# Optimization experiments

Hardware: AMD Instinct MI355X
Metric: run time of the kernel (lower is better)

## Reference

```python
import jax, jax.numpy as jnp
import numpy as np

Z_DIM = 2
N_STEPS = 4  # fixed-step RK4 stand-in for adaptive dopri5 over t in [0, 1]


def _mlp(t, z, W1, b1, W2, b2, W3, b3):
    # get_z_dot: concat time column before every layer, softplus between layers
    h = z
    params = ((W1, b1), (W2, b2), (W3, b3))
    for i, (W, b) in enumerate(params):
        tcol = jnp.full((h.shape[0], 1), t, dtype=h.dtype)
        h = jnp.concatenate([tcol, h], axis=1) @ W.T + b
        if i < len(params) - 1:
            h = jax.nn.softplus(h)
    return h


def _dynamics(t, z, params):
    # z_dot = NN(t, z); exact divergence = trace of dz_dot/dz via JVPs with basis vectors
    f = lambda zz: _mlp(t, zz, *params)
    div = jnp.zeros((z.shape[0],), dtype=z.dtype)
    z_dot = None
    for i in range(Z_DIM):
        e = jnp.zeros_like(z).at[:, i].set(1.0)
        primal, jv = jax.jvp(f, (z,), (e,))
        z_dot = primal
        div = div + jv[:, i]
    return z_dot, -div[:, None]


def _integrate(z, delta_logpz, params):
    dt = 1.0 / N_STEPS
    f = lambda tt, zz: _dynamics(tt, zz, params)

    def step(carry, i):
        zc, lc = carry
        t = i * dt
        k1z, k1l = f(t, zc)
        k2z, k2l = f(t + 0.5 * dt, zc + 0.5 * dt * k1z)
        k3z, k3l = f(t + 0.5 * dt, zc + 0.5 * dt * k2z)
        k4z, k4l = f(t + dt, zc + dt * k3z)
        zn = zc + (dt / 6.0) * (k1z + 2.0 * k2z + 2.0 * k3z + k4z)
        ln = lc + (dt / 6.0) * (k1l + 2.0 * k2l + 2.0 * k3l + k4l)
        return (zn, ln), None

    (zf, lf), _ = jax.lax.scan(step, (z, delta_logpz), jnp.arange(N_STEPS, dtype=z.dtype))
    return zf, lf


def setup_inputs() -> dict:
    key = jax.random.key(0)
    ks = jax.random.split(key, 4)
    B = 262144
    z = jax.random.normal(ks[0], (B, Z_DIM), dtype=jnp.float32)
    delta_logpz = jnp.zeros((B, 1), dtype=jnp.float32)
    # Linear layers: in_dim + 1 for time column
    W1 = jax.random.normal(ks[1], (64, Z_DIM + 1), dtype=jnp.float32) * (1.0 / np.sqrt(Z_DIM + 1))
    b1 = jnp.zeros((64,), dtype=jnp.float32)
    W2 = jax.random.normal(ks[2], (64, 64 + 1), dtype=jnp.float32) * (1.0 / np.sqrt(65))
    b2 = jnp.zeros((64,), dtype=jnp.float32)
    W3 = jax.random.normal(ks[3], (Z_DIM, 64 + 1), dtype=jnp.float32) * (1.0 / np.sqrt(65))
    b3 = jnp.zeros((Z_DIM,), dtype=jnp.float32)
    return {"z": z, "delta_logpz": delta_logpz, "W1": W1, "b1": b1, "W2": W2, "b2": b2, "W3": W3, "b3": b3}


def reference(z, delta_logpz, W1, b1, W2, b2, W3, b3):
    params = (W1, b1, W2, b2, W3, b3)
    return _integrate(z, delta_logpz, params)
```

## Files before the change

kernel.cpp:

```cpp
#include <hip/hip_runtime.h>

#define HDIM 64
#define NSTEPS 4

typedef __attribute__((ext_vector_type(4))) float f32x4;
typedef __attribute__((ext_vector_type(8))) short bf16x8;
typedef unsigned int uint;

union FragU { uint u[4]; uint4 u4; bf16x8 v; };

__device__ inline uint cvt_pk_bf16(float a, float b) {
  uint d;
  asm("v_cvt_pk_bf16_f32 %0, %1, %2" : "=v"(d) : "v"(a), "v"(b));
  return d;
}
__device__ inline float lo_bf16_f32(uint p) { return __builtin_bit_cast(float, p << 16); }
__device__ inline float hi_bf16_f32(uint p) { return __builtin_bit_cast(float, p & 0xFFFF0000u); }

__device__ inline unsigned short rne_bf16u(float x) {
  uint u = __builtin_bit_cast(uint, x);
  uint r = u + 0x7FFFu + ((u >> 16) & 1u);
  return (unsigned short)(r >> 16);
}
__device__ inline float bf16f(unsigned short h) { return __builtin_bit_cast(float, ((uint)h) << 16); }

__device__ inline float row_sum16(float x) {
  int v = __builtin_bit_cast(int, x);
  x += __builtin_bit_cast(float, __builtin_amdgcn_update_dpp(0, v, 0x128, 0xF, 0xF, true));
  v = __builtin_bit_cast(int, x);
  x += __builtin_bit_cast(float, __builtin_amdgcn_update_dpp(0, v, 0x124, 0xF, 0xF, true));
  v = __builtin_bit_cast(int, x);
  x += __builtin_bit_cast(float, __builtin_amdgcn_update_dpp(0, v, 0x122, 0xF, 0xF, true));
  v = __builtin_bit_cast(int, x);
  x += __builtin_bit_cast(float, __builtin_amdgcn_update_dpp(0, v, 0x121, 0xF, 0xF, true));
  return x;
}

__device__ inline void pack2(float x0, float x1, uint& H, uint& L) {
  uint h = cvt_pk_bf16(x0, x1);
  H = h;
  L = cvt_pk_bf16(x0 - lo_bf16_f32(h), x1 - hi_bf16_f32(h));
}

__device__ inline void l1chain(float4 par, float base, float s0, float s1,
                               float& sp, float& sg) {
  float a = fmaf(par.y, s0, fmaf(par.z, s1, base));
  float ex = __expf(-fabsf(a));
  float rc = __builtin_amdgcn_rcpf(1.0f + ex);
  sg = (a >= 0.f ? 1.0f : ex) * rc;
  sp = fmaxf(a, 0.f) + __logf(1.0f + ex);
}


__global__ void ffjord_prep(const float* __restrict__ W1, const float* __restrict__ b1,
                            const float* __restrict__ W2, const float* __restrict__ b2,
                            const float* __restrict__ W3, const float* __restrict__ b3,
                            float* __restrict__ ws) {
  int tid = threadIdx.x;
  uint* wsu = (uint*)ws;
  for (int e2 = tid; e2 < 8192; e2 += 256) {
    int mat = e2 >> 11;
    int rem = e2 & 2047;
    int fr  = rem >> 8;
    int l   = (rem >> 2) & 63;
    int d   = rem & 3;
    int kt = fr >> 2, nt = fr & 3;
    int g = l >> 4, cc = l & 15;
    int k0 = kt * 32 + g * 8 + 2 * d;
    int j  = nt * 16 + cc;
    float v0, v1;
    if (mat < 2) {
      v0 = W2[j * 65 + k0 + 1];
      v1 = W2[j * 65 + k0 + 2];
    } else {
      float p0 = W1[k0 * 3 + 1] * W3[j + 1] + W1[k0 * 3 + 2] * W3[65 + j + 1];
      float p1 = W1[(k0 + 1) * 3 + 1] * W3[j + 1] + W1[(k0 + 1) * 3 + 2] * W3[65 + j + 1];
      v0 = p0 * W2[j * 65 + k0 + 1];
      v1 = p1 * W2[j * 65 + k0 + 2];
    }
    unsigned short h0 = rne_bf16u(v0), h1 = rne_bf16u(v1);
    if (mat & 1) {
      h0 = rne_bf16u(v0 - bf16f(rne_bf16u(v0)));
      h1 = rne_bf16u(v1 - bf16f(rne_bf16u(v1)));
    }
    wsu[e2] = (uint)h0 | ((uint)h1 << 16);
  }
  if (tid < HDIM) {
    ws[8192 + tid * 4 + 0] = W1[tid * 3 + 0];
    ws[8192 + tid * 4 + 1] = W1[tid * 3 + 1];
    ws[8192 + tid * 4 + 2] = W1[tid * 3 + 2];
    ws[8192 + tid * 4 + 3] = b1[tid];
    ws[8448 + tid * 2 + 0] = W2[tid * 65 + 0];
    ws[8448 + tid * 2 + 1] = b2[tid];
    ws[8576 + tid * 2 + 0] = W3[tid + 1];
    ws[8576 + tid * 2 + 1] = W3[65 + tid + 1];
  }
  if (tid == 0) {
    ws[8704] = W3[0];
    ws[8705] = W3[65];
    ws[8706] = b3[0];
    ws[8707] = b3[1];
  }
}

__global__ __launch_bounds__(256, 2) void ffjord_main(
    const float* __restrict__ z_in, const float* __restrict__ dlp_in,
    const float* __restrict__ ws, float* __restrict__ out, int B) {
  __shared__ uint4 fragLds[2048];
  __shared__ float4 l1Lds[64];
  __shared__ float2 c2Lds[64];
  __shared__ float2 l3Lds[64];
  __shared__ float  redLds[4][3][64];

  int tid = threadIdx.x;
  const uint4* wsu4 = (const uint4*)ws;
  #pragma unroll
  for (int j = 0; j < 8; ++j) fragLds[tid + 256 * j] = wsu4[tid + 256 * j];
  if (tid < 64) {
    l1Lds[tid] = ((const float4*)(ws + 8192))[tid];
    c2Lds[tid] = ((const float2*)(ws + 8448))[tid];
    l3Lds[tid] = ((const float2*)(ws + 8576))[tid];
  }
  __syncthreads();

  const float c30 = ws[8704], c31 = ws[8705], cb0 = ws[8706], cb1 = ws[8707];

  int wid = tid >> 6, l = tid & 63;
  int g = l >> 4, c = l & 15;
  int pt = blockIdx.x * 256 + wid * 64 + l;
  int ptc = pt < B ? pt : (B - 1);

  float z0 = z_in[2 * ptc], z1 = z_in[2 * ptc + 1];
  float lp = dlp_in[ptc];
  const float dt = 1.0f / NSTEPS;

  #pragma unroll 1
  for (int step = 0; step < NSTEPS; ++step) {
    float t0 = step * dt;
    float az0 = 0.f, az1 = 0.f, al = 0.f;
    float zt0 = z0, zt1 = z1, ts = t0;

    #pragma unroll 1
    for (int s = 0; s < 4; ++s) {
      float c2n[4];
      #pragma unroll
      for (int nt = 0; nt < 4; ++nt) {
        float2 cc = c2Lds[nt * 16 + c];
        c2n[nt] = fmaf(cc.x, ts, cc.y);
      }

      #pragma unroll 1
      for (int p = 0; p < 2; ++p) {
        asm volatile("" ::: "memory");
        int mtA = 2 * p, mtB = 2 * p + 1;
        float sA0 = __shfl(zt0, mtA * 16 + c);
        float sA1 = __shfl(zt1, mtA * 16 + c);
        float sB0 = __shfl(zt0, mtB * 16 + c);
        float sB1 = __shfl(zt1, mtB * 16 + c);

        FragU SPhA[2], SPlA[2], SGhA[2], SGlA[2];
        FragU SPhB[2], SPlB[2], SGhB[2], SGlB[2];
        #pragma unroll
        for (int kt = 0; kt < 2; ++kt) {
          #pragma unroll
          for (int d = 0; d < 4; ++d) {
            float4 p0 = l1Lds[kt * 32 + g * 8 + 2 * d];
            float4 p1 = l1Lds[kt * 32 + g * 8 + 2 * d + 1];
            float b0 = fmaf(p0.x, ts, p0.w);
            float b1 = fmaf(p1.x, ts, p1.w);
            float spA0, sgA0, spA1, sgA1, spB0, sgB0, spB1, sgB1;
            l1chain(p0, b0, sA0, sA1, spA0, sgA0);
            l1chain(p1, b1, sA0, sA1, spA1, sgA1);
            l1chain(p0, b0, sB0, sB1, spB0, sgB0);
            l1chain(p1, b1, sB0, sB1, spB1, sgB1);
            pack2(spA0, spA1, SPhA[kt].u[d], SPlA[kt].u[d]);
            pack2(sgA0, sgA1, SGhA[kt].u[d], SGlA[kt].u[d]);
            pack2(spB0, spB1, SPhB[kt].u[d], SPlB[kt].u[d]);
            pack2(sgB0, sgB1, SGhB[kt].u[d], SGlB[kt].u[d]);
          }
        }

        f32x4 C1A[4], C1B[4];
        #pragma unroll
        for (int nt = 0; nt < 4; ++nt) {
          C1A[nt] = (f32x4){0.f, 0.f, 0.f, 0.f};
          C1B[nt] = (f32x4){0.f, 0.f, 0.f, 0.f};
        }
        #pragma unroll
        for (int kt = 0; kt < 2; ++kt) {
          #pragma unroll
          for (int nt = 0; nt < 4; ++nt) {
            FragU Bh, Bl;
            Bh.u4 = fragLds[(kt * 4 + nt) * 64 + l];
            Bl.u4 = fragLds[512 + (kt * 4 + nt) * 64 + l];
            C1A[nt] = __builtin_amdgcn_mfma_f32_16x16x32_bf16(SPhA[kt].v, Bh.v, C1A[nt], 0, 0, 0);
            C1B[nt] = __builtin_amdgcn_mfma_f32_16x16x32_bf16(SPhB[kt].v, Bh.v, C1B[nt], 0, 0, 0);
            C1A[nt] = __builtin_amdgcn_mfma_f32_16x16x32_bf16(SPhA[kt].v, Bl.v, C1A[nt], 0, 0, 0);
            C1B[nt] = __builtin_amdgcn_mfma_f32_16x16x32_bf16(SPhB[kt].v, Bl.v, C1B[nt], 0, 0, 0);
            C1A[nt] = __builtin_amdgcn_mfma_f32_16x16x32_bf16(SPlA[kt].v, Bh.v, C1A[nt], 0, 0, 0);
            C1B[nt] = __builtin_amdgcn_mfma_f32_16x16x32_bf16(SPlB[kt].v, Bh.v, C1B[nt], 0, 0, 0);
          }
        }

        float zp0A[4] = {0.f, 0.f, 0.f, 0.f}, zp1A[4] = {0.f, 0.f, 0.f, 0.f};
        float zp0B[4] = {0.f, 0.f, 0.f, 0.f}, zp1B[4] = {0.f, 0.f, 0.f, 0.f};
        float gA[4][4], gB[4][4];
        #pragma unroll
        for (int nt = 0; nt < 4; ++nt) {
          float2 l3 = l3Lds[nt * 16 + c];
          #pragma unroll
          for (int r = 0; r < 4; ++r) {
            {
              float h2 = C1A[nt][r] + c2n[nt];
              float ex = __expf(-fabsf(h2));
              float rc = __builtin_amdgcn_rcpf(1.0f + ex);
              gA[nt][r] = (h2 >= 0.f ? 1.0f : ex) * rc;
              float sq = fmaxf(h2, 0.f) + __logf(1.0f + ex);
              zp0A[r] = fmaf(l3.x, sq, zp0A[r]);
              zp1A[r] = fmaf(l3.y, sq, zp1A[r]);
            }
            {
              float h2 = C1B[nt][r] + c2n[nt];
              float ex = __expf(-fabsf(h2));
              float rc = __builtin_amdgcn_rcpf(1.0f + ex);
              gB[nt][r] = (h2 >= 0.f ? 1.0f : ex) * rc;
              float sq = fmaxf(h2, 0.f) + __logf(1.0f + ex);
              zp0B[r] = fmaf(l3.x, sq, zp0B[r]);
              zp1B[r] = fmaf(l3.y, sq, zp1B[r]);
            }
          }
        }
        #pragma unroll
        for (int r = 0; r < 4; ++r) {
          zp0A[r] = row_sum16(zp0A[r]); zp1A[r] = row_sum16(zp1A[r]);
          zp0B[r] = row_sum16(zp0B[r]); zp1B[r] = row_sum16(zp1B[r]);
        }
        if (c == 0) {
          #pragma unroll
          for (int r = 0; r < 4; ++r) {
            redLds[wid][0][mtA * 16 + g * 4 + r] = zp0A[r];
            redLds[wid][1][mtA * 16 + g * 4 + r] = zp1A[r];
            redLds[wid][0][mtB * 16 + g * 4 + r] = zp0B[r];
            redLds[wid][1][mtB * 16 + g * 4 + r] = zp1B[r];
          }
        }

        float dvA[4] = {0.f, 0.f, 0.f, 0.f}, dvB[4] = {0.f, 0.f, 0.f, 0.f};
        #pragma unroll
        for (int nt = 0; nt < 4; ++nt) {
          f32x4 C2A = (f32x4){0.f, 0.f, 0.f, 0.f};
          f32x4 C2B = (f32x4){0.f, 0.f, 0.f, 0.f};
          #pragma unroll
          for (int kt = 0; kt < 2; ++kt) {
            FragU Bh, Bl;
            Bh.u4 = fragLds[1024 + (kt * 4 + nt) * 64 + l];
            Bl.u4 = fragLds[1536 + (kt * 4 + nt) * 64 + l];
            C2A = __builtin_amdgcn_mfma_f32_16x16x32_bf16(SGhA[kt].v, Bh.v, C2A, 0, 0, 0);
            C2B = __builtin_amdgcn_mfma_f32_16x16x32_bf16(SGhB[kt].v, Bh.v, C2B, 0, 0, 0);
            C2A = __builtin_amdgcn_mfma_f32_16x16x32_bf16(SGhA[kt].v, Bl.v, C2A, 0, 0, 0);
            C2B = __builtin_amdgcn_mfma_f32_16x16x32_bf16(SGhB[kt].v, Bl.v, C2B, 0, 0, 0);
            C2A = __builtin_amdgcn_mfma_f32_16x16x32_bf16(SGlA[kt].v, Bh.v, C2A, 0, 0, 0);
            C2B = __builtin_amdgcn_mfma_f32_16x16x32_bf16(SGlB[kt].v, Bh.v, C2B, 0, 0, 0);
          }
          #pragma unroll
          for (int r = 0; r < 4; ++r) {
            dvA[r] = fmaf(C2A[r], gA[nt][r], dvA[r]);
            dvB[r] = fmaf(C2B[r], gB[nt][r], dvB[r]);
          }
        }
        #pragma unroll
        for (int r = 0; r < 4; ++r) {
          dvA[r] = row_sum16(dvA[r]);
          dvB[r] = row_sum16(dvB[r]);
        }
        if (c == 0) {
          #pragma unroll
          for (int r = 0; r < 4; ++r) {
            redLds[wid][2][mtA * 16 + g * 4 + r] = dvA[r];
            redLds[wid][2][mtB * 16 + g * 4 + r] = dvB[r];
          }
        }
      }

      float zd0 = redLds[wid][0][l] + fmaf(c30, ts, cb0);
      float zd1 = redLds[wid][1][l] + fmaf(c31, ts, cb1);
      float dv  = redLds[wid][2][l];

      float w = (s == 1 || s == 2) ? 2.0f : 1.0f;
      az0 = fmaf(w, zd0, az0);
      az1 = fmaf(w, zd1, az1);
      al  = fmaf(w, dv, al);
      if (s < 3) {
        float cc2 = (s == 2) ? dt : 0.5f * dt;
        zt0 = fmaf(cc2, zd0, z0);
        zt1 = fmaf(cc2, zd1, z1);
        ts = t0 + cc2;
      }
    }
    z0 = fmaf(dt / 6.0f, az0, z0);
    z1 = fmaf(dt / 6.0f, az1, z1);
    lp = fmaf(-dt / 6.0f, al, lp);
  }

  if (pt < B) {
    out[2 * pt] = z0;
    out[2 * pt + 1] = z1;
    out[2 * B + pt] = lp;
  }
}

extern "C" void kernel_launch(void* const* d_in, const int* in_sizes, int n_in,
                              void* d_out, int out_size, void* d_ws, size_t ws_size,
                              hipStream_t stream) {
  const float* z   = (const float*)d_in[0];
  const float* dlp = (const float*)d_in[1];
  const float* W1  = (const float*)d_in[2];
  const float* b1  = (const float*)d_in[3];
  const float* W2  = (const float*)d_in[4];
  const float* b2  = (const float*)d_in[5];
  const float* W3  = (const float*)d_in[6];
  const float* b3  = (const float*)d_in[7];
  float* out = (float*)d_out;
  float* ws = (float*)d_ws;

  int B = in_sizes[0] / 2;

  ffjord_prep<<<1, 256, 0, stream>>>(W1, b1, W2, b2, W3, b3, ws);
  int blocks = (B + 255) / 256;
  ffjord_main<<<blocks, 256, 0, stream>>>(z, dlp, ws, out, B);
}
```

Baseline: 601.7 us.

## Defer divergence row-reduction to after all RK4 steps

Divergence partials are no longer cross-lane reduced and written to LDS at every stage. They are accumulated per lane with RK4 weights across all steps and stages, then reduced once at the end, which is valid because the reduction is linear. This removes many row_sum16 shuffles and LDS round trips from the inner loop. The cost is 16 extra live accumulator registers, so launch bounds drop from 2 to 1 blocks per CU to allow more registers, which may reduce occupancy.

```diff
diff --git a/kernel.cpp b/kernel.cpp
--- a/kernel.cpp
+++ b/kernel.cpp
@@ -103,14 +103,14 @@
   }
 }
 
-__global__ __launch_bounds__(256, 2) void ffjord_main(
+__global__ __launch_bounds__(256, 1) void ffjord_main(
     const float* __restrict__ z_in, const float* __restrict__ dlp_in,
     const float* __restrict__ ws, float* __restrict__ out, int B) {
   __shared__ uint4 fragLds[2048];
   __shared__ float4 l1Lds[64];
   __shared__ float2 c2Lds[64];
   __shared__ float2 l3Lds[64];
-  __shared__ float  redLds[4][3][64];
+  __shared__ float  redLds[4][2][64];
 
   int tid = threadIdx.x;
   const uint4* wsu4 = (const uint4*)ws;
@@ -134,14 +134,18 @@
   float lp = dlp_in[ptc];
   const float dt = 1.0f / NSTEPS;
 
+  float acc0A[4] = {0.f, 0.f, 0.f, 0.f}, acc0B[4] = {0.f, 0.f, 0.f, 0.f};
+  float acc1A[4] = {0.f, 0.f, 0.f, 0.f}, acc1B[4] = {0.f, 0.f, 0.f, 0.f};
+
   #pragma unroll 1
   for (int step = 0; step < NSTEPS; ++step) {
     float t0 = step * dt;
-    float az0 = 0.f, az1 = 0.f, al = 0.f;
+    float az0 = 0.f, az1 = 0.f;
     float zt0 = z0, zt1 = z1, ts = t0;
 
     #pragma unroll 1
     for (int s = 0; s < 4; ++s) {
+      float w = (s == 1 || s == 2) ? 2.0f : 1.0f;
       float c2n[4];
       #pragma unroll
       for (int nt = 0; nt < 4; ++nt) {
@@ -268,28 +272,26 @@
             dvB[r] = fmaf(C2B[r], gB[nt][r], dvB[r]);
           }
         }
-        #pragma unroll
-        for (int r = 0; r < 4; ++r) {
-          dvA[r] = row_sum16(dvA[r]);
-          dvB[r] = row_sum16(dvB[r]);
-        }
-        if (c == 0) {
-          #pragma unroll
-          for (int r = 0; r < 4; ++r) {
-            redLds[wid][2][mtA * 16 + g * 4 + r] = dvA[r];
-            redLds[wid][2][mtB * 16 + g * 4 + r] = dvB[r];
+        if (p == 0) {
+          #pragma unroll
+          for (int r = 0; r < 4; ++r) {
+            acc0A[r] = fmaf(w, dvA[r], acc0A[r]);
+            acc0B[r] = fmaf(w, dvB[r], acc0B[r]);
+          }
+        } else {
+          #pragma unroll
+          for (int r = 0; r < 4; ++r) {
+            acc1A[r] = fmaf(w, dvA[r], acc1A[r]);
+            acc1B[r] = fmaf(w, dvB[r], acc1B[r]);
           }
         }
       }
 
       float zd0 = redLds[wid][0][l] + fmaf(c30, ts, cb0);
       float zd1 = redLds[wid][1][l] + fmaf(c31, ts, cb1);
-      float dv  = redLds[wid][2][l];
-
-      float w = (s == 1 || s == 2) ? 2.0f : 1.0f;
+
       az0 = fmaf(w, zd0, az0);
       az1 = fmaf(w, zd1, az1);
-      al  = fmaf(w, dv, al);
       if (s < 3) {
         float cc2 = (s == 2) ? dt : 0.5f * dt;
         zt0 = fmaf(cc2, zd0, z0);
@@ -299,8 +301,26 @@
     }
     z0 = fmaf(dt / 6.0f, az0, z0);
     z1 = fmaf(dt / 6.0f, az1, z1);
-    lp = fmaf(-dt / 6.0f, al, lp);
-  }
+  }
+
+  #pragma unroll
+  for (int r = 0; r < 4; ++r) {
+    acc0A[r] = row_sum16(acc0A[r]);
+    acc0B[r] = row_sum16(acc0B[r]);
+    acc1A[r] = row_sum16(acc1A[r]);
+    acc1B[r] = row_sum16(acc1B[r]);
+  }
+  if (c == 0) {
+    #pragma unroll
+    for (int r = 0; r < 4; ++r) {
+      redLds[wid][0][0 * 16 + g * 4 + r] = acc0A[r];
+      redLds[wid][0][1 * 16 + g * 4 + r] = acc0B[r];
+      redLds[wid][0][2 * 16 + g * 4 + r] = acc1A[r];
+      redLds[wid][0][3 * 16 + g * 4 + r] = acc1B[r];
+    }
+  }
+  float alTot = redLds[wid][0][l];
+  lp = fmaf(-dt / 6.0f, alTot, lp);
 
   if (pt < B) {
     out[2 * pt] = z0;
```

After: 681.0 us. 13.2% more time.
